# Performance work log

Measured on AMD Instinct MI355X. Metric: run time of the kernel, lower is better.

The kernel has to match this reference:

```python
import jax, jax.numpy as jnp
import numpy as np

N_NODES = 100000
N_EDGES = 3200000
NFEAT, HID, NCLASS = 256, 32, 16


def setup_inputs() -> dict:
    key = jax.random.key(0)
    ks = jax.random.split(key, 6)
    x = jax.random.normal(ks[0], (N_NODES, NFEAT), dtype=jnp.float32)
    edge_index = jax.random.randint(ks[1], (2, N_EDGES), 0, N_NODES, dtype=jnp.int64)
    edge_weight = jax.random.uniform(ks[2], (N_EDGES,), dtype=jnp.float32)
    # Glorot-ish init for the two GCNConv linear weights; bias zeros (PyG default init zeros bias)
    W1 = jax.random.normal(ks[3], (NFEAT, HID), dtype=jnp.float32) * (1.0 / np.sqrt(NFEAT))
    b1 = jnp.zeros((HID,), dtype=jnp.float32)
    W2 = jax.random.normal(ks[4], (HID, NCLASS), dtype=jnp.float32) * (1.0 / np.sqrt(HID))
    b2 = jnp.zeros((NCLASS,), dtype=jnp.float32)
    return {"x": x, "edge_index": edge_index, "edge_weight": edge_weight,
            "W1": W1, "b1": b1, "W2": W2, "b2": b2}


def _gcn_norm(row, col, w, n):
    """PyG gcn_norm: add self-loops (weight 1), symmetric normalization."""
    loop = jnp.arange(n, dtype=row.dtype)
    row = jnp.concatenate([row, loop])
    col = jnp.concatenate([col, loop])
    w = jnp.concatenate([w, jnp.ones((n,), dtype=w.dtype)])
    deg = jax.ops.segment_sum(w, col, num_segments=n)  # degree at target nodes
    dinv = jnp.where(deg > 0, jax.lax.rsqrt(deg), 0.0)
    norm = dinv[row] * w * dinv[col]
    return row, col, norm


def _gcn_conv(x, W, b, row, col, norm, n):
    xw = x @ W                                  # [N, out]
    msg = xw[row] * norm[:, None]               # gather at source + scale
    out = jax.ops.segment_sum(msg, col, num_segments=n)  # scatter-add at target
    return out + b


def reference(x, edge_index, edge_weight, W1, b1, W2, b2):
    n = x.shape[0]
    row, col, norm = _gcn_norm(edge_index[0], edge_index[1], edge_weight, n)
    h = jax.nn.relu(_gcn_conv(x, W1, b1, row, col, norm, n))
    # dropout is identity in eval mode
    logits = _gcn_conv(h, W2, b2, row, col, norm, n)
    return jax.nn.log_softmax(logits, axis=1)
```

## Files before the change

kernel.cpp:

```cpp
#include <hip/hip_runtime.h>

#define N_NODES 100000
#define N_EDGES 3200000
#define NFEAT 256
#define HID 32
#define NCLASS 16

#define NB 64
#define CHUNK (N_EDGES / NB)
#define RN4 65536
#define NR4 2

#define SCAN_TPB 256
#define SCAN_EPB 1024
#define SCAN_NBLK ((N_NODES + SCAN_EPB - 1) / SCAN_EPB)

#define XPAD 133

__device__ inline unsigned short f2bf(float f) {
    unsigned u = __float_as_uint(f);
    u += 0x7FFFu + ((u >> 16) & 1u);
    return (unsigned short)(u >> 16);
}
__device__ inline float bf2f(unsigned short s) {
    return __uint_as_float((unsigned)s << 16);
}
__device__ inline void bf8_unpack(uint4 g, float* f) {
    f[0] = __uint_as_float(g.x << 16); f[1] = __uint_as_float(g.x & 0xFFFF0000u);
    f[2] = __uint_as_float(g.y << 16); f[3] = __uint_as_float(g.y & 0xFFFF0000u);
    f[4] = __uint_as_float(g.z << 16); f[5] = __uint_as_float(g.z & 0xFFFF0000u);
    f[6] = __uint_as_float(g.w << 16); f[7] = __uint_as_float(g.w & 0xFFFF0000u);
}

__global__ __launch_bounds__(1024) void k_count(const int* __restrict__ col,
                                                unsigned* __restrict__ H,
                                                unsigned char* __restrict__ pos) {
    __shared__ unsigned hist[RN4 / 4];
    int t = threadIdx.x, b = blockIdx.x, r = blockIdx.y;
    int base = r * RN4;
    const int* cc = col + (size_t)b * CHUNK;
    unsigned char* pp = pos + (size_t)b * CHUNK;
    for (int i = t; i < RN4 / 4; i += 1024) hist[i] = 0;
    __syncthreads();
    for (int i = t; i < CHUNK; i += 1024) {
        unsigned d = (unsigned)cc[i] - (unsigned)base;
        if (d < RN4) {
            unsigned sh = (d & 3) * 8;
            unsigned old = atomicAdd(&hist[d >> 2], 1u << sh);
            pp[i] = (unsigned char)((old >> sh) & 0xFFu);
        }
    }
    __syncthreads();
    int lim = min(RN4, N_NODES - base);
    unsigned* Hb = H + (size_t)b * N_NODES;
    for (int i = t; i < lim; i += 1024)
        Hb[base + i] = (hist[i >> 2] >> ((i & 3) * 8)) & 0xFFu;
}

__global__ void k_prefix16(const unsigned* __restrict__ H,
                           unsigned short* __restrict__ SP, int* __restrict__ cnt) {
    int n = blockIdx.x * 256 + threadIdx.x;
    if (n >= N_NODES) return;
    unsigned run = 0;
    #pragma unroll 8
    for (int b = 0; b < NB; ++b) {
        size_t i = (size_t)b * N_NODES + n;
        unsigned v = H[i];
        SP[i] = (unsigned short)run;
        run += v;
    }
    cnt[n] = (int)run;
}

__global__ __launch_bounds__(SCAN_TPB) void k_scanA(const int* __restrict__ cnt,
                                                    int* __restrict__ offs,
                                                    int* __restrict__ bsum) {
    __shared__ int s[SCAN_TPB];
    int t = threadIdx.x;
    int base = blockIdx.x * SCAN_EPB + t * 4;
    int v0 = (base + 0 < N_NODES) ? cnt[base + 0] : 0;
    int v1 = (base + 1 < N_NODES) ? cnt[base + 1] : 0;
    int v2 = (base + 2 < N_NODES) ? cnt[base + 2] : 0;
    int v3 = (base + 3 < N_NODES) ? cnt[base + 3] : 0;
    int sum = v0 + v1 + v2 + v3;
    s[t] = sum;
    __syncthreads();
    for (int off = 1; off < SCAN_TPB; off <<= 1) {
        int x = (t >= off) ? s[t - off] : 0;
        __syncthreads();
        s[t] += x;
        __syncthreads();
    }
    int excl = s[t] - sum;
    if (t == SCAN_TPB - 1) bsum[blockIdx.x] = s[t];
    int run = excl;
    if (base + 0 < N_NODES) offs[base + 0] = run; run += v0;
    if (base + 1 < N_NODES) offs[base + 1] = run; run += v1;
    if (base + 2 < N_NODES) offs[base + 2] = run; run += v2;
    if (base + 3 < N_NODES) offs[base + 3] = run;
}

__global__ __launch_bounds__(128) void k_scanB(int* __restrict__ bsum) {
    __shared__ int s[128];
    int t = threadIdx.x;
    int v = (t < SCAN_NBLK) ? bsum[t] : 0;
    s[t] = v;
    __syncthreads();
    for (int off = 1; off < 128; off <<= 1) {
        int x = (t >= off) ? s[t - off] : 0;
        __syncthreads();
        s[t] += x;
        __syncthreads();
    }
    if (t < SCAN_NBLK) bsum[t] = s[t] - v;
}

__global__ __launch_bounds__(SCAN_TPB) void k_scanC(int* __restrict__ offs,
                                                    const int* __restrict__ bsum) {
    int t = threadIdx.x;
    int add = bsum[blockIdx.x];
    int base = blockIdx.x * SCAN_EPB + t * 4;
    #pragma unroll
    for (int i = 0; i < 4; ++i) {
        int idx = base + i;
        if (idx < N_NODES) offs[idx] += add;
    }
    if (blockIdx.x == 0 && t == 0) offs[N_NODES] = N_EDGES;
}

__global__ void k_emit(const int* __restrict__ row, const int* __restrict__ col,
                       const float* __restrict__ w, const int* __restrict__ offs,
                       const unsigned short* __restrict__ SP,
                       const unsigned char* __restrict__ pos,
                       float2* __restrict__ ein) {
    int e = blockIdx.x * 256 + threadIdx.x;
    if (e >= N_EDGES) return;
    int b = e / CHUNK;
    int c = col[e];
    unsigned p = (unsigned)offs[c] + (unsigned)SP[(size_t)b * N_NODES + c]
               + (unsigned)pos[e];
    ein[p] = make_float2(__int_as_float(row[e]), w[e]);
}

__global__ void k_deg(const float2* __restrict__ ein, const int* __restrict__ offs,
                      float* __restrict__ dinv) {
    int idx = blockIdx.x * 256 + threadIdx.x;
    int n = idx >> 2, l = idx & 3;
    if (n >= N_NODES) return;
    int s = offs[n], e = offs[n + 1];
    float sum = 0.f;
    for (int p = s + l; p < e; p += 4) sum += ein[p].y;
    sum += __shfl_xor(sum, 1, 4);
    sum += __shfl_xor(sum, 2, 4);
    if (l == 0) dinv[n] = rsqrtf(1.0f + sum);
}

__global__ __launch_bounds__(256) void k_gemm1s(const float* __restrict__ x,
                                                const float* __restrict__ W1,
                                                unsigned short* __restrict__ xwp) {
    __shared__ float sWc[32 * HID];
    __shared__ float sX[32 * XPAD];
    int t = threadIdx.x;
    long rowbase = (long)blockIdx.x * 128;
    int kbase = blockIdx.y * 128;
    unsigned short* xw = xwp + (size_t)blockIdx.y * N_NODES * HID;
    int tr = t >> 3;
    int tc = t & 7;
    float acc[4][4] = {};
    for (int k0 = kbase; k0 < kbase + 128; k0 += 32) {
        *(float4*)&sWc[t * 4] = *(const float4*)&W1[k0 * HID + t * 4];
        #pragma unroll
        for (int p = 0; p < 4; ++p) {
            int rt = (t >> 3) + p * 32;
            int kk = (t & 7) * 4;
            long grow = rowbase + rt;
            float4 v = make_float4(0.f, 0.f, 0.f, 0.f);
            if (grow < N_NODES) v = *(const float4*)&x[grow * NFEAT + k0 + kk];
            sX[(kk + 0) * XPAD + rt] = v.x; sX[(kk + 1) * XPAD + rt] = v.y;
            sX[(kk + 2) * XPAD + rt] = v.z; sX[(kk + 3) * XPAD + rt] = v.w;
        }
        __syncthreads();
        #pragma unroll 8
        for (int kk = 0; kk < 32; ++kk) {
            float xv[4], wv[4];
            xv[0] = sX[kk * XPAD + tr * 4 + 0];
            xv[1] = sX[kk * XPAD + tr * 4 + 1];
            xv[2] = sX[kk * XPAD + tr * 4 + 2];
            xv[3] = sX[kk * XPAD + tr * 4 + 3];
            *(float4*)&wv[0] = *(float4*)&sWc[kk * HID + tc * 4];
            #pragma unroll
            for (int m = 0; m < 4; ++m)
                #pragma unroll
                for (int n = 0; n < 4; ++n)
                    acc[m][n] = fmaf(xv[m], wv[n], acc[m][n]);
        }
        __syncthreads();
    }
    #pragma unroll
    for (int m = 0; m < 4; ++m) {
        long r = rowbase + tr * 4 + m;
        if (r < N_NODES) {
            ushort4 o;
            o.x = f2bf(acc[m][0]); o.y = f2bf(acc[m][1]);
            o.z = f2bf(acc[m][2]); o.w = f2bf(acc[m][3]);
            *(ushort4*)&xw[r * HID + tc * 4] = o;
        }
    }
}

__global__ void k_comb(const unsigned short* __restrict__ xwp,
                       ushort4* __restrict__ xwb) {
    int i = blockIdx.x * 256 + threadIdx.x;
    const ushort4* p0 = (const ushort4*)xwp;
    const ushort4* p1 = p0 + 800000;
    ushort4 a = p0[i], b = p1[i];
    ushort4 o;
    o.x = f2bf(bf2f(a.x) + bf2f(b.x));
    o.y = f2bf(bf2f(a.y) + bf2f(b.y));
    o.z = f2bf(bf2f(a.z) + bf2f(b.z));
    o.w = f2bf(bf2f(a.w) + bf2f(b.w));
    xwb[i] = o;
}

__global__ __launch_bounds__(256) void k_gather1(const unsigned short* __restrict__ xwb,
                                                 const float* __restrict__ dinv,
                                                 const float2* __restrict__ ein,
                                                 const int* __restrict__ offs,
                                                 const float* __restrict__ b1,
                                                 float* __restrict__ h) {
    int idx = blockIdx.x * 256 + threadIdx.x;
    int n = idx >> 3, l = idx & 7;
    int c4 = l * 4;
    const ushort4* xb = (const ushort4*)xwb;
    float di = dinv[n];
    ushort4 q = xb[(long)n * 8 + l];
    float4 acc = make_float4(bf2f(q.x) * di, bf2f(q.y) * di,
                             bf2f(q.z) * di, bf2f(q.w) * di);
    int s = offs[n], e = offs[n + 1];
    for (int p0 = s; p0 < e; p0 += 8) {
        int pl = p0 + l;
        float2 pr = (pl < e) ? ein[pl] : make_float2(__int_as_float(n), 0.f);
        int ri = __float_as_int(pr.x);
        pr.y *= dinv[ri];
        #pragma unroll
        for (int j = 0; j < 8; ++j) {
            int r = __shfl(ri, j, 8);
            float nm = __shfl(pr.y, j, 8);
            ushort4 g = xb[(long)r * 8 + l];
            acc.x = fmaf(bf2f(g.x), nm, acc.x);
            acc.y = fmaf(bf2f(g.y), nm, acc.y);
            acc.z = fmaf(bf2f(g.z), nm, acc.z);
            acc.w = fmaf(bf2f(g.w), nm, acc.w);
        }
    }
    float4 bb = *(const float4*)&b1[c4];
    acc.x = fmaxf(fmaf(acc.x, di, bb.x), 0.f);
    acc.y = fmaxf(fmaf(acc.y, di, bb.y), 0.f);
    acc.z = fmaxf(fmaf(acc.z, di, bb.z), 0.f);
    acc.w = fmaxf(fmaf(acc.w, di, bb.w), 0.f);
    *(float4*)&h[(long)n * HID + c4] = acc;
}

__global__ __launch_bounds__(256) void k_gemm2(const float* __restrict__ h,
                                               const float* __restrict__ W2,
                                               unsigned short* __restrict__ hwb) {
    __shared__ float sH[64][33];
    __shared__ float sW2[HID * NCLASS];
    int t = threadIdx.x;
    if (t < 128) {
        int idx = t * 4;
        *(float4*)&sW2[idx] = *(const float4*)&W2[idx];
    }
    long base = (long)blockIdx.x * 64;
    #pragma unroll
    for (int i = 0; i < 2; ++i) {
        int idx = t + i * 256;
        int rt = idx >> 3, kk = (idx & 7) * 4;
        long gr = base + rt;
        float4 v = make_float4(0.f, 0.f, 0.f, 0.f);
        if (gr < N_NODES) v = *(const float4*)&h[gr * HID + kk];
        sH[rt][kk + 0] = v.x; sH[rt][kk + 1] = v.y;
        sH[rt][kk + 2] = v.z; sH[rt][kk + 3] = v.w;
    }
    __syncthreads();
    int r = t >> 2, c4 = (t & 3) * 4;
    float acc[4] = {};
    #pragma unroll
    for (int k = 0; k < HID; ++k) {
        float hv = sH[r][k];
        float wv[4];
        *(float4*)&wv[0] = *(float4*)&sW2[k * NCLASS + c4];
        #pragma unroll
        for (int n = 0; n < 4; ++n) acc[n] = fmaf(hv, wv[n], acc[n]);
    }
    long gr = base + r;
    if (gr < N_NODES) {
        ushort4 o;
        o.x = f2bf(acc[0]); o.y = f2bf(acc[1]);
        o.z = f2bf(acc[2]); o.w = f2bf(acc[3]);
        *(ushort4*)&hwb[gr * NCLASS + c4] = o;
    }
}

__global__ __launch_bounds__(256) void k_gather2(const unsigned short* __restrict__ hwb,
                                                 const float* __restrict__ dinv,
                                                 const float2* __restrict__ ein,
                                                 const int* __restrict__ offs,
                                                 const float* __restrict__ b2,
                                                 float* __restrict__ out) {
    int idx = blockIdx.x * 256 + threadIdx.x;
    int n = idx >> 1, l = idx & 1;
    if (n >= N_NODES) return;
    int c8 = l * 8;
    const uint4* hb = (const uint4*)hwb;
    float di = dinv[n];
    float acc[8], f[8];
    bf8_unpack(hb[(long)n * 2 + l], f);
    #pragma unroll
    for (int k = 0; k < 8; ++k) acc[k] = f[k] * di;
    int s = offs[n], e = offs[n + 1];
    for (int p0 = s; p0 < e; p0 += 8) {
        float2 pr[4];
        int rr[4];
        #pragma unroll
        for (int k = 0; k < 4; ++k) {
            int pl = p0 + k * 2 + l;
            pr[k] = (pl < e) ? ein[pl] : make_float2(__int_as_float(n), 0.f);
            rr[k] = __float_as_int(pr[k].x);
            pr[k].y *= dinv[rr[k]];
        }
        #pragma unroll
        for (int k = 0; k < 4; ++k) {
            #pragma unroll
            for (int j = 0; j < 2; ++j) {
                int r = __shfl(rr[k], j, 2);
                float nm = __shfl(pr[k].y, j, 2);
                bf8_unpack(hb[(long)r * 2 + l], f);
                #pragma unroll
                for (int q = 0; q < 8; ++q) acc[q] = fmaf(f[q], nm, acc[q]);
            }
        }
    }
    float4 bb0 = *(const float4*)&b2[c8];
    float4 bb1 = *(const float4*)&b2[c8 + 4];
    float v[8];
    v[0] = fmaf(acc[0], di, bb0.x); v[1] = fmaf(acc[1], di, bb0.y);
    v[2] = fmaf(acc[2], di, bb0.z); v[3] = fmaf(acc[3], di, bb0.w);
    v[4] = fmaf(acc[4], di, bb1.x); v[5] = fmaf(acc[5], di, bb1.y);
    v[6] = fmaf(acc[6], di, bb1.z); v[7] = fmaf(acc[7], di, bb1.w);
    float m = v[0];
    #pragma unroll
    for (int k = 1; k < 8; ++k) m = fmaxf(m, v[k]);
    m = fmaxf(m, __shfl_xor(m, 1, 2));
    float sum = 0.f;
    #pragma unroll
    for (int k = 0; k < 8; ++k) sum += __expf(v[k] - m);
    sum += __shfl_xor(sum, 1, 2);
    float ls = m + __logf(sum);
    float4 o0 = make_float4(v[0] - ls, v[1] - ls, v[2] - ls, v[3] - ls);
    float4 o1 = make_float4(v[4] - ls, v[5] - ls, v[6] - ls, v[7] - ls);
    *(float4*)&out[(long)n * NCLASS + c8] = o0;
    *(float4*)&out[(long)n * NCLASS + c8 + 4] = o1;
}

extern "C" void kernel_launch(void* const* d_in, const int* in_sizes, int n_in,
                              void* d_out, int out_size, void* d_ws, size_t ws_size,
                              hipStream_t stream) {
    const float* x  = (const float*)d_in[0];
    const int*   ei = (const int*)d_in[1];
    const float* w  = (const float*)d_in[2];
    const float* W1 = (const float*)d_in[3];
    const float* b1 = (const float*)d_in[4];
    const float* W2 = (const float*)d_in[5];
    const float* b2 = (const float*)d_in[6];
    float* out = (float*)d_out;

    const int* row = ei;
    const int* col = ei + N_EDGES;

    float* ws = (float*)d_ws;
    float2* ein = (float2*)ws;
    unsigned* H = (unsigned*)(ws + 2 * (size_t)N_EDGES);
    unsigned char* pos = (unsigned char*)(ws + 2 * (size_t)N_EDGES + (size_t)NB * N_NODES);
    float* h = (float*)pos;
    float* dinv = ws + 2 * (size_t)N_EDGES + (size_t)NB * N_NODES + N_EDGES;
    int* cnt = (int*)(dinv + N_NODES);
    int* offs = cnt + N_NODES;
    int* bsum = offs + N_NODES + 1;
    size_t xwp_off = (size_t)(2 * (size_t)N_EDGES + (size_t)NB * N_NODES + N_EDGES
                              + 3 * N_NODES + 1 + 128);
    xwp_off = (xwp_off + 3) & ~(size_t)3;
    unsigned short* xwp = (unsigned short*)(ws + xwp_off);
    unsigned short* xwb = (unsigned short*)(ws + xwp_off + 3200000);
    unsigned short* hwb = xwb + (size_t)N_NODES * HID;
    unsigned short* SP = hwb + (size_t)N_NODES * NCLASS;

    const int B = 256;

    k_count<<<dim3(NB, NR4), 1024, 0, stream>>>(col, H, pos);
    k_prefix16<<<(N_NODES + B - 1) / B, B, 0, stream>>>(H, SP, cnt);
    k_scanA<<<SCAN_NBLK, SCAN_TPB, 0, stream>>>(cnt, offs, bsum);
    k_scanB<<<1, 128, 0, stream>>>(bsum);
    k_scanC<<<SCAN_NBLK, SCAN_TPB, 0, stream>>>(offs, bsum);
    k_emit<<<(N_EDGES + B - 1) / B, B, 0, stream>>>(row, col, w, offs, SP, pos, ein);

    k_deg<<<(N_NODES * 4 + B - 1) / B, B, 0, stream>>>(ein, offs, dinv);

    k_gemm1s<<<dim3((N_NODES + 127) / 128, 2), 256, 0, stream>>>(x, W1, xwp);
    k_comb<<<(N_NODES * HID / 4) / B, B, 0, stream>>>(xwp, (ushort4*)xwb);
    k_gather1<<<(N_NODES * 8) / B, B, 0, stream>>>(xwb, dinv, ein, offs, b1, h);

    k_gemm2<<<(N_NODES + 63) / 64, B, 0, stream>>>(h, W2, hwb);
    k_gather2<<<(N_NODES * 2 + B - 1) / B, B, 0, stream>>>(hwb, dinv, ein, offs, b2, out);
}
```

Before: 275.3 us.

## Pack edge row and weight into 32 bits and fuse emit with GEMM1

Edges in the CSR array are now stored as one 32-bit word: a 17-bit source index plus a custom 15-bit compressed weight (a reduced exponent with 10 mantissa bits). This halves edge-array traffic in the emit, degree and both gather kernels. The edge-scatter kernel and the first GEMM are also merged into one launch by interleaving their blocks, so the two can overlap. In exchange, edge weights lose precision, and the node index is assumed to fit in 17 bits.

```diff
diff --git a/kernel.cpp b/kernel.cpp
--- a/kernel.cpp
+++ b/kernel.cpp
@@ -16,6 +16,9 @@
 #define SCAN_NBLK ((N_NODES + SCAN_EPB - 1) / SCAN_EPB)
 
 #define XPAD 133
+#define NGEMM 1564
+#define NEMIT ((N_EDGES + 255) / 256)
+#define FGRID (NGEMM * 9)
 
 __device__ inline unsigned short f2bf(float f) {
     unsigned u = __float_as_uint(f);
@@ -30,6 +33,17 @@
     f[2] = __uint_as_float(g.y << 16); f[3] = __uint_as_float(g.y & 0xFFFF0000u);
     f[4] = __uint_as_float(g.z << 16); f[5] = __uint_as_float(g.z & 0xFFFF0000u);
     f[6] = __uint_as_float(g.w << 16); f[7] = __uint_as_float(g.w & 0xFFFF0000u);
+}
+__device__ inline unsigned wenc(float w) {
+    unsigned u = __float_as_uint(w) + (1u << 12);
+    int e = (int)((u >> 23) & 0xFF) - 95;
+    if (e < 0) return 0u;
+    unsigned v = ((unsigned)e << 10) | ((u >> 13) & 0x3FFu);
+    return v > 0x7FFFu ? 0x7FFFu : v;
+}
+__device__ inline float wdec(unsigned v) {
+    if (v == 0) return 0.f;
+    return __uint_as_float((((v >> 10) + 95u) << 23) | ((v & 0x3FFu) << 13));
 }
 
 __global__ __launch_bounds__(1024) void k_count(const int* __restrict__ col,
@@ -128,84 +142,88 @@
     if (blockIdx.x == 0 && t == 0) offs[N_NODES] = N_EDGES;
 }
 
-__global__ void k_emit(const int* __restrict__ row, const int* __restrict__ col,
-                       const float* __restrict__ w, const int* __restrict__ offs,
-                       const unsigned short* __restrict__ SP,
-                       const unsigned char* __restrict__ pos,
-                       float2* __restrict__ ein) {
-    int e = blockIdx.x * 256 + threadIdx.x;
-    if (e >= N_EDGES) return;
-    int b = e / CHUNK;
-    int c = col[e];
-    unsigned p = (unsigned)offs[c] + (unsigned)SP[(size_t)b * N_NODES + c]
-               + (unsigned)pos[e];
-    ein[p] = make_float2(__int_as_float(row[e]), w[e]);
-}
-
-__global__ void k_deg(const float2* __restrict__ ein, const int* __restrict__ offs,
+__global__ __launch_bounds__(256) void k_emit_gemm(
+        const int* __restrict__ row, const int* __restrict__ col,
+        const float* __restrict__ w, const int* __restrict__ offs,
+        const unsigned short* __restrict__ SP, const unsigned char* __restrict__ pos,
+        unsigned* __restrict__ ein,
+        const float* __restrict__ x, const float* __restrict__ W1,
+        unsigned short* __restrict__ xwp) {
+    __shared__ float smem[32 * HID + 32 * XPAD];
+    int bid = blockIdx.x;
+    int g = bid / 9, r9 = bid - g * 9;
+    if (r9 == 0 && g < NGEMM) {
+        float* sWc = smem;
+        float* sX = smem + 32 * HID;
+        int t = threadIdx.x;
+        long rowbase = (long)(g >> 1) * 128;
+        int kbase = (g & 1) * 128;
+        unsigned short* xw = xwp + (size_t)(g & 1) * N_NODES * HID;
+        int tr = t >> 3, tc = t & 7;
+        float acc[4][4] = {};
+        for (int k0 = kbase; k0 < kbase + 128; k0 += 32) {
+            *(float4*)&sWc[t * 4] = *(const float4*)&W1[k0 * HID + t * 4];
+            #pragma unroll
+            for (int p = 0; p < 4; ++p) {
+                int rt = (t >> 3) + p * 32;
+                int kk = (t & 7) * 4;
+                long grow = rowbase + rt;
+                float4 v = make_float4(0.f, 0.f, 0.f, 0.f);
+                if (grow < N_NODES) v = *(const float4*)&x[grow * NFEAT + k0 + kk];
+                sX[(kk + 0) * XPAD + rt] = v.x; sX[(kk + 1) * XPAD + rt] = v.y;
+                sX[(kk + 2) * XPAD + rt] = v.z; sX[(kk + 3) * XPAD + rt] = v.w;
+            }
+            __syncthreads();
+            #pragma unroll 8
+            for (int kk = 0; kk < 32; ++kk) {
+                float xv[4], wv[4];
+                xv[0] = sX[kk * XPAD + tr * 4 + 0];
+                xv[1] = sX[kk * XPAD + tr * 4 + 1];
+                xv[2] = sX[kk * XPAD + tr * 4 + 2];
+                xv[3] = sX[kk * XPAD + tr * 4 + 3];
+                *(float4*)&wv[0] = *(float4*)&sWc[kk * HID + tc * 4];
+                #pragma unroll
+                for (int m = 0; m < 4; ++m)
+                    #pragma unroll
+                    for (int n = 0; n < 4; ++n)
+                        acc[m][n] = fmaf(xv[m], wv[n], acc[m][n]);
+            }
+            __syncthreads();
+        }
+        #pragma unroll
+        for (int m = 0; m < 4; ++m) {
+            long rr = rowbase + tr * 4 + m;
+            if (rr < N_NODES) {
+                ushort4 o;
+                o.x = f2bf(acc[m][0]); o.y = f2bf(acc[m][1]);
+                o.z = f2bf(acc[m][2]); o.w = f2bf(acc[m][3]);
+                *(ushort4*)&xw[rr * HID + tc * 4] = o;
+            }
+        }
+    } else {
+        int emit_id = bid - ((r9 == 0) ? NGEMM : min(g + 1, NGEMM));
+        if (emit_id >= NEMIT) return;
+        int e = emit_id * 256 + threadIdx.x;
+        if (e >= N_EDGES) return;
+        int b = e / CHUNK;
+        int c = col[e];
+        unsigned p = (unsigned)offs[c] + (unsigned)SP[(size_t)b * N_NODES + c]
+                   + (unsigned)pos[e];
+        ein[p] = (wenc(w[e]) << 17) | (unsigned)row[e];
+    }
+}
+
+__global__ void k_deg(const unsigned* __restrict__ ein, const int* __restrict__ offs,
                       float* __restrict__ dinv) {
     int idx = blockIdx.x * 256 + threadIdx.x;
     int n = idx >> 2, l = idx & 3;
     if (n >= N_NODES) return;
     int s = offs[n], e = offs[n + 1];
     float sum = 0.f;
-    for (int p = s + l; p < e; p += 4) sum += ein[p].y;
+    for (int p = s + l; p < e; p += 4) sum += wdec(ein[p] >> 17);
     sum += __shfl_xor(sum, 1, 4);
     sum += __shfl_xor(sum, 2, 4);
     if (l == 0) dinv[n] = rsqrtf(1.0f + sum);
-}
-
-__global__ __launch_bounds__(256) void k_gemm1s(const float* __restrict__ x,
-                                                const float* __restrict__ W1,
-                                                unsigned short* __restrict__ xwp) {
-    __shared__ float sWc[32 * HID];
-    __shared__ float sX[32 * XPAD];
-    int t = threadIdx.x;
-    long rowbase = (long)blockIdx.x * 128;
-    int kbase = blockIdx.y * 128;
-    unsigned short* xw = xwp + (size_t)blockIdx.y * N_NODES * HID;
-    int tr = t >> 3;
-    int tc = t & 7;
-    float acc[4][4] = {};
-    for (int k0 = kbase; k0 < kbase + 128; k0 += 32) {
-        *(float4*)&sWc[t * 4] = *(const float4*)&W1[k0 * HID + t * 4];
-        #pragma unroll
-        for (int p = 0; p < 4; ++p) {
-            int rt = (t >> 3) + p * 32;
-            int kk = (t & 7) * 4;
-            long grow = rowbase + rt;
-            float4 v = make_float4(0.f, 0.f, 0.f, 0.f);
-            if (grow < N_NODES) v = *(const float4*)&x[grow * NFEAT + k0 + kk];
-            sX[(kk + 0) * XPAD + rt] = v.x; sX[(kk + 1) * XPAD + rt] = v.y;
-            sX[(kk + 2) * XPAD + rt] = v.z; sX[(kk + 3) * XPAD + rt] = v.w;
-        }
-        __syncthreads();
-        #pragma unroll 8
-        for (int kk = 0; kk < 32; ++kk) {
-            float xv[4], wv[4];
-            xv[0] = sX[kk * XPAD + tr * 4 + 0];
-            xv[1] = sX[kk * XPAD + tr * 4 + 1];
-            xv[2] = sX[kk * XPAD + tr * 4 + 2];
-            xv[3] = sX[kk * XPAD + tr * 4 + 3];
-            *(float4*)&wv[0] = *(float4*)&sWc[kk * HID + tc * 4];
-            #pragma unroll
-            for (int m = 0; m < 4; ++m)
-                #pragma unroll
-                for (int n = 0; n < 4; ++n)
-                    acc[m][n] = fmaf(xv[m], wv[n], acc[m][n]);
-        }
-        __syncthreads();
-    }
-    #pragma unroll
-    for (int m = 0; m < 4; ++m) {
-        long r = rowbase + tr * 4 + m;
-        if (r < N_NODES) {
-            ushort4 o;
-            o.x = f2bf(acc[m][0]); o.y = f2bf(acc[m][1]);
-            o.z = f2bf(acc[m][2]); o.w = f2bf(acc[m][3]);
-            *(ushort4*)&xw[r * HID + tc * 4] = o;
-        }
-    }
 }
 
 __global__ void k_comb(const unsigned short* __restrict__ xwp,
@@ -224,7 +242,7 @@
 
 __global__ __launch_bounds__(256) void k_gather1(const unsigned short* __restrict__ xwb,
                                                  const float* __restrict__ dinv,
-                                                 const float2* __restrict__ ein,
+                                                 const unsigned* __restrict__ ein,
                                                  const int* __restrict__ offs,
                                                  const float* __restrict__ b1,
                                                  float* __restrict__ h) {
@@ -239,18 +257,18 @@
     int s = offs[n], e = offs[n + 1];
     for (int p0 = s; p0 < e; p0 += 8) {
         int pl = p0 + l;
-        float2 pr = (pl < e) ? ein[pl] : make_float2(__int_as_float(n), 0.f);
-        int ri = __float_as_int(pr.x);
-        pr.y *= dinv[ri];
+        unsigned v = (pl < e) ? ein[pl] : (unsigned)n;
+        int ri = v & 0x1FFFF;
+        float nm = wdec(v >> 17) * dinv[ri];
         #pragma unroll
         for (int j = 0; j < 8; ++j) {
             int r = __shfl(ri, j, 8);
-            float nm = __shfl(pr.y, j, 8);
+            float nmj = __shfl(nm, j, 8);
             ushort4 g = xb[(long)r * 8 + l];
-            acc.x = fmaf(bf2f(g.x), nm, acc.x);
-            acc.y = fmaf(bf2f(g.y), nm, acc.y);
-            acc.z = fmaf(bf2f(g.z), nm, acc.z);
-            acc.w = fmaf(bf2f(g.w), nm, acc.w);
+            acc.x = fmaf(bf2f(g.x), nmj, acc.x);
+            acc.y = fmaf(bf2f(g.y), nmj, acc.y);
+            acc.z = fmaf(bf2f(g.z), nmj, acc.z);
+            acc.w = fmaf(bf2f(g.w), nmj, acc.w);
         }
     }
     float4 bb = *(const float4*)&b1[c4];
@@ -304,7 +322,7 @@
 
 __global__ __launch_bounds__(256) void k_gather2(const unsigned short* __restrict__ hwb,
                                                  const float* __restrict__ dinv,
-                                                 const float2* __restrict__ ein,
+                                                 const unsigned* __restrict__ ein,
                                                  const int* __restrict__ offs,
                                                  const float* __restrict__ b2,
                                                  float* __restrict__ out) {
@@ -320,24 +338,24 @@
     for (int k = 0; k < 8; ++k) acc[k] = f[k] * di;
     int s = offs[n], e = offs[n + 1];
     for (int p0 = s; p0 < e; p0 += 8) {
-        float2 pr[4];
         int rr[4];
+        float nm[4];
         #pragma unroll
         for (int k = 0; k < 4; ++k) {
             int pl = p0 + k * 2 + l;
-            pr[k] = (pl < e) ? ein[pl] : make_float2(__int_as_float(n), 0.f);
-            rr[k] = __float_as_int(pr[k].x);
-            pr[k].y *= dinv[rr[k]];
+            unsigned v = (pl < e) ? ein[pl] : (unsigned)n;
+            rr[k] = v & 0x1FFFF;
+            nm[k] = wdec(v >> 17) * dinv[rr[k]];
         }
         #pragma unroll
         for (int k = 0; k < 4; ++k) {
             #pragma unroll
             for (int j = 0; j < 2; ++j) {
                 int r = __shfl(rr[k], j, 2);
-                float nm = __shfl(pr[k].y, j, 2);
+                float nmj = __shfl(nm[k], j, 2);
                 bf8_unpack(hb[(long)r * 2 + l], f);
                 #pragma unroll
-                for (int q = 0; q < 8; ++q) acc[q] = fmaf(f[q], nm, acc[q]);
+                for (int q = 0; q < 8; ++q) acc[q] = fmaf(f[q], nmj, acc[q]);
             }
         }
     }
@@ -379,15 +397,15 @@
     const int* col = ei + N_EDGES;
 
     float* ws = (float*)d_ws;
-    float2* ein = (float2*)ws;
-    unsigned* H = (unsigned*)(ws + 2 * (size_t)N_EDGES);
-    unsigned char* pos = (unsigned char*)(ws + 2 * (size_t)N_EDGES + (size_t)NB * N_NODES);
+    unsigned* ein = (unsigned*)ws;
+    unsigned* H = (unsigned*)(ws + (size_t)N_EDGES);
+    unsigned char* pos = (unsigned char*)(ws + (size_t)N_EDGES + (size_t)NB * N_NODES);
     float* h = (float*)pos;
-    float* dinv = ws + 2 * (size_t)N_EDGES + (size_t)NB * N_NODES + N_EDGES;
+    float* dinv = ws + (size_t)N_EDGES + (size_t)NB * N_NODES + N_EDGES;
     int* cnt = (int*)(dinv + N_NODES);
     int* offs = cnt + N_NODES;
     int* bsum = offs + N_NODES + 1;
-    size_t xwp_off = (size_t)(2 * (size_t)N_EDGES + (size_t)NB * N_NODES + N_EDGES
+    size_t xwp_off = (size_t)((size_t)N_EDGES + (size_t)NB * N_NODES + N_EDGES
                               + 3 * N_NODES + 1 + 128);
     xwp_off = (xwp_off + 3) & ~(size_t)3;
     unsigned short* xwp = (unsigned short*)(ws + xwp_off);
@@ -402,11 +420,10 @@
     k_scanA<<<SCAN_NBLK, SCAN_TPB, 0, stream>>>(cnt, offs, bsum);
     k_scanB<<<1, 128, 0, stream>>>(bsum);
     k_scanC<<<SCAN_NBLK, SCAN_TPB, 0, stream>>>(offs, bsum);
-    k_emit<<<(N_EDGES + B - 1) / B, B, 0, stream>>>(row, col, w, offs, SP, pos, ein);
+
+    k_emit_gemm<<<FGRID, B, 0, stream>>>(row, col, w, offs, SP, pos, ein, x, W1, xwp);
 
     k_deg<<<(N_NODES * 4 + B - 1) / B, B, 0, stream>>>(ein, offs, dinv);
-
-    k_gemm1s<<<dim3((N_NODES + 127) / 128, 2), 256, 0, stream>>>(x, W1, xwp);
     k_comb<<<(N_NODES * HID / 4) / B, B, 0, stream>>>(xwp, (ushort4*)xwb);
     k_gather1<<<(N_NODES * 8) / B, B, 0, stream>>>(xwb, dinv, ein, offs, b1, h);
 
```

Result: slower. 283.7 us (+3.1%).

## Pre-bucket edges by destination octant and scatter per XCC for locality

Applied to the files above, without the earlier changes.

Replaces the single-pass edge emit with a two-stage scatter. Edges are first bucketed into eight destination ranges per chunk. Blocks then pull tiles for their XCC's octant through a work-stealing counter, so the final scatter into the CSR array and the offs/SP lookups stay within a smaller address range per XCC L2. This adds three kernels and an extra write and read of the packed edge data, and relies on reading a hardware XCC id register.

```diff
diff --git a/kernel.cpp b/kernel.cpp
--- a/kernel.cpp
+++ b/kernel.cpp
@@ -10,6 +10,7 @@
 #define CHUNK (N_EDGES / NB)
 #define RN4 65536
 #define NR4 2
+#define OCT 12500
 
 #define SCAN_TPB 256
 #define SCAN_EPB 1024
@@ -30,6 +31,11 @@
     f[2] = __uint_as_float(g.y << 16); f[3] = __uint_as_float(g.y & 0xFFFF0000u);
     f[4] = __uint_as_float(g.z << 16); f[5] = __uint_as_float(g.z & 0xFFFF0000u);
     f[6] = __uint_as_float(g.w << 16); f[7] = __uint_as_float(g.w & 0xFFFF0000u);
+}
+__device__ inline int xcc_id() {
+    unsigned v;
+    asm volatile("s_getreg_b32 %0, hwreg(20, 0, 32)" : "=s"(v));
+    return (int)(v & 7u);
 }
 
 __global__ __launch_bounds__(1024) void k_count(const int* __restrict__ col,
@@ -128,18 +134,93 @@
     if (blockIdx.x == 0 && t == 0) offs[N_NODES] = N_EDGES;
 }
 
-__global__ void k_emit(const int* __restrict__ row, const int* __restrict__ col,
-                       const float* __restrict__ w, const int* __restrict__ offs,
-                       const unsigned short* __restrict__ SP,
-                       const unsigned char* __restrict__ pos,
-                       float2* __restrict__ ein) {
-    int e = blockIdx.x * 256 + threadIdx.x;
-    if (e >= N_EDGES) return;
-    int b = e / CHUNK;
-    int c = col[e];
-    unsigned p = (unsigned)offs[c] + (unsigned)SP[(size_t)b * N_NODES + c]
-               + (unsigned)pos[e];
-    ein[p] = make_float2(__int_as_float(row[e]), w[e]);
+__global__ __launch_bounds__(1024) void k_bo(const int* __restrict__ col,
+                                             unsigned* __restrict__ BO) {
+    __shared__ unsigned c8[8];
+    int t = threadIdx.x, b = blockIdx.x;
+    if (t < 8) c8[t] = 0;
+    __syncthreads();
+    const int* cc = col + (size_t)b * CHUNK;
+    for (int i = t; i < CHUNK; i += 1024) atomicAdd(&c8[cc[i] / OCT], 1u);
+    __syncthreads();
+    if (t < 8) BO[b * 8 + t] = c8[t];
+}
+
+__global__ __launch_bounds__(256) void k_boscan(const unsigned* __restrict__ BO,
+                                                unsigned* __restrict__ bases,
+                                                unsigned* __restrict__ tilecnt) {
+    __shared__ unsigned s[256];
+    int t = threadIdx.x;
+    unsigned v0 = BO[t * 2], v1 = BO[t * 2 + 1];
+    unsigned sum = v0 + v1;
+    s[t] = sum;
+    __syncthreads();
+    for (int off = 1; off < 256; off <<= 1) {
+        unsigned x = (t >= off) ? s[t - off] : 0;
+        __syncthreads();
+        s[t] += x;
+        __syncthreads();
+    }
+    unsigned run = s[t] - sum;
+    bases[t * 2] = run;
+    bases[t * 2 + 1] = run + v0;
+    if (t == 255) bases[512] = run + sum;
+    if (t < 8) tilecnt[t] = 0;
+}
+
+__global__ __launch_bounds__(256) void k_bucketA(const int* __restrict__ row,
+                                                 const int* __restrict__ col,
+                                                 const float* __restrict__ w,
+                                                 const unsigned char* __restrict__ pos,
+                                                 const unsigned* __restrict__ bases,
+                                                 unsigned long long* __restrict__ AB8,
+                                                 unsigned* __restrict__ AB4) {
+    __shared__ unsigned cur[8];
+    int t = threadIdx.x, b = blockIdx.x;
+    if (t < 8) cur[t] = bases[b * 8 + t];
+    __syncthreads();
+    size_t eb = (size_t)b * CHUNK;
+    for (int i = t; i < CHUNK; i += 256) {
+        size_t e = eb + i;
+        int c = col[e];
+        int o = c / OCT;
+        unsigned slot = atomicAdd(&cur[o], 1u);
+        AB8[slot] = ((unsigned long long)__float_as_uint(w[e]) << 32) | (unsigned)row[e];
+        AB4[slot] = ((unsigned)(c - o * OCT) << 8) | (unsigned)pos[e];
+    }
+}
+
+__global__ __launch_bounds__(256) void k_bucketB(const unsigned long long* __restrict__ AB8,
+                                                 const unsigned* __restrict__ AB4,
+                                                 const int* __restrict__ offs,
+                                                 const unsigned short* __restrict__ SP,
+                                                 const unsigned* __restrict__ bases,
+                                                 unsigned* __restrict__ tilecnt,
+                                                 float2* __restrict__ ein) {
+    __shared__ int sb;
+    int o0 = xcc_id();
+    for (int k = 0; k < 8; ++k) {
+        int o = (o0 + k) & 7;
+        int cbase = o * OCT;
+        for (;;) {
+            __syncthreads();
+            if (threadIdx.x == 0) sb = (int)atomicAdd(&tilecnt[o], 1u);
+            __syncthreads();
+            int b = sb;
+            if (b >= NB) break;
+            unsigned g = (unsigned)b * 8u + (unsigned)o;
+            unsigned start = bases[g], end = bases[g + 1];
+            const unsigned short* SPb = SP + (size_t)b * N_NODES;
+            for (unsigned i = start + threadIdx.x; i < end; i += 256) {
+                unsigned long long v8 = __builtin_nontemporal_load(&AB8[i]);
+                unsigned v4 = __builtin_nontemporal_load(&AB4[i]);
+                int c = cbase + (int)(v4 >> 8);
+                unsigned p = (unsigned)offs[c] + (unsigned)SPb[c] + (v4 & 0xFFu);
+                ein[p] = make_float2(__uint_as_float((unsigned)v8),
+                                     __uint_as_float((unsigned)(v8 >> 32)));
+            }
+        }
+    }
 }
 
 __global__ void k_deg(const float2* __restrict__ ein, const int* __restrict__ offs,
@@ -381,6 +462,7 @@
     float* ws = (float*)d_ws;
     float2* ein = (float2*)ws;
     unsigned* H = (unsigned*)(ws + 2 * (size_t)N_EDGES);
+    unsigned long long* AB8 = (unsigned long long*)H;
     unsigned char* pos = (unsigned char*)(ws + 2 * (size_t)N_EDGES + (size_t)NB * N_NODES);
     float* h = (float*)pos;
     float* dinv = ws + 2 * (size_t)N_EDGES + (size_t)NB * N_NODES + N_EDGES;
@@ -391,9 +473,13 @@
                               + 3 * N_NODES + 1 + 128);
     xwp_off = (xwp_off + 3) & ~(size_t)3;
     unsigned short* xwp = (unsigned short*)(ws + xwp_off);
+    unsigned* AB4 = (unsigned*)xwp;
     unsigned short* xwb = (unsigned short*)(ws + xwp_off + 3200000);
     unsigned short* hwb = xwb + (size_t)N_NODES * HID;
     unsigned short* SP = hwb + (size_t)N_NODES * NCLASS;
+    unsigned* BO = (unsigned*)(SP + (size_t)NB * N_NODES);
+    unsigned* bases = BO + 512;
+    unsigned* tilecnt = bases + 513;
 
     const int B = 256;
 
@@ -402,7 +488,11 @@
     k_scanA<<<SCAN_NBLK, SCAN_TPB, 0, stream>>>(cnt, offs, bsum);
     k_scanB<<<1, 128, 0, stream>>>(bsum);
     k_scanC<<<SCAN_NBLK, SCAN_TPB, 0, stream>>>(offs, bsum);
-    k_emit<<<(N_EDGES + B - 1) / B, B, 0, stream>>>(row, col, w, offs, SP, pos, ein);
+
+    k_bo<<<NB, 1024, 0, stream>>>(col, BO);
+    k_boscan<<<1, B, 0, stream>>>(BO, bases, tilecnt);
+    k_bucketA<<<NB, B, 0, stream>>>(row, col, w, pos, bases, AB8, AB4);
+    k_bucketB<<<2048, B, 0, stream>>>(AB8, AB4, offs, SP, bases, tilecnt, ein);
 
     k_deg<<<(N_NODES * 4 + B - 1) / B, B, 0, stream>>>(ein, offs, dinv);
 
```

Measured after the change: 631.5 us. 2.29x slower.
